# Optimization experiments

Hardware: AMD Instinct MI355X
Metric: run time of the kernel (lower is better)

The kernel has to match this reference:

```python
import jax, jax.numpy as jnp
import numpy as np

S, D, H, DK, DV = 2048, 1024, 16, 64, 64


def setup_inputs() -> dict:
    key = jax.random.key(0)
    ks = jax.random.split(key, 7)
    sc = 1.0 / np.sqrt(D)
    return {
        "encodings_for_q": jax.random.normal(ks[0], (S, D), jnp.float32),
        "encodings_for_k": jax.random.normal(ks[1], (S, D), jnp.float32),
        "encodings_for_v": jax.random.normal(ks[2], (S, D), jnp.float32),
        # per-head projection weights, stacked over heads (math-equivalent to
        # num_heads separate bias-free nn.Linear layers)
        "W_q": jax.random.normal(ks[3], (H, D, DK), jnp.float32) * sc,
        "W_k": jax.random.normal(ks[4], (H, D, DK), jnp.float32) * sc,
        "W_v": jax.random.normal(ks[5], (H, D, DV), jnp.float32) * sc,
        "W_out": jax.random.normal(ks[6], (H * DV, D), jnp.float32) * sc,
    }


def reference(encodings_for_q, encodings_for_k, encodings_for_v, W_q, W_k, W_v, W_out):
    # per-head projections: [H, S, dk/dv]
    q = jnp.einsum("sd,hdk->hsk", encodings_for_q, W_q)
    k = jnp.einsum("sd,hdk->hsk", encodings_for_k, W_k)
    v = jnp.einsum("sd,hdv->hsv", encodings_for_v, W_v)
    # scaled dot-product attention; scale = sqrt(d_k) (k.size(col_dim))
    sims = jnp.einsum("hsk,htk->hst", q, k) / jnp.sqrt(jnp.asarray(DK, q.dtype))
    attn = jax.nn.softmax(sims, axis=-1)
    ctx = jnp.einsum("hst,htv->hsv", attn, v)  # [H, S, dv]
    # concat heads along feature dim (head-major order, like torch.cat)
    cat = jnp.transpose(ctx, (1, 0, 2)).reshape(S, H * DV)
    return cat @ W_out
```

## Files before the change

kernel.cpp:

```cpp
#include <hip/hip_runtime.h>
#include <hip/hip_bf16.h>

typedef __attribute__((ext_vector_type(8))) short bf16x8;
typedef __attribute__((ext_vector_type(4))) float f32x4;

#define S_  2048
#define D_  1024
#define H_  16
#define QK_SCALE 0.18033688011f

__device__ __forceinline__ unsigned short f2bf(float x) {
    union { float f; unsigned u; } v; v.f = x;
    unsigned r = v.u + 0x7fffu + ((v.u >> 16) & 1u);
    return (unsigned short)(r >> 16);
}

__device__ __forceinline__ float bf2f(unsigned short s) {
    union { unsigned u; float f; } v; v.u = (unsigned)s << 16; return v.f;
}

__device__ __forceinline__ unsigned short bfbits(float x) {
    union { __hip_bfloat16 h; unsigned short s; } c;
    c.h = __float2bfloat16(x);
    return c.s;
}

__device__ __forceinline__ float fm3(float a, float b, float c) {
    return fmaxf(fmaxf(a, b), c);
}

__device__ __forceinline__ void gload16(const unsigned short* g, unsigned short* l) {
    __builtin_amdgcn_global_load_lds((const __attribute__((address_space(1))) void*)g,
                                     (__attribute__((address_space(3))) void*)l, 16, 0, 0);
}

__device__ __forceinline__ void drain_vm() {
    asm volatile("s_waitcnt vmcnt(0)" ::: "memory");
}

__global__ __launch_bounds__(256) void prep(
    const float* __restrict__ eq, const float* __restrict__ ek, const float* __restrict__ ev,
    const float* __restrict__ wq, const float* __restrict__ wk, const float* __restrict__ wv,
    const float* __restrict__ wo,
    unsigned short* __restrict__ oeq, unsigned short* __restrict__ oek,
    unsigned short* __restrict__ oev, unsigned short* __restrict__ owq,
    unsigned short* __restrict__ owk, unsigned short* __restrict__ owv,
    unsigned short* __restrict__ owo) {
    const int bx = blockIdx.x, tid = threadIdx.x;
    if (bx < 6144) {
        const float* in = bx < 2048 ? eq : bx < 4096 ? ek : ev;
        unsigned short* out = bx < 2048 ? oeq : bx < 4096 ? oek : oev;
        int i = (bx & 2047) * 256 + tid;
        float4 v = ((const float4*)in)[i];
        ushort4 o;
        o.x = f2bf(v.x); o.y = f2bf(v.y); o.z = f2bf(v.z); o.w = f2bf(v.w);
        ((ushort4*)out)[i] = o;
        return;
    }
    __shared__ float t[32][33];
    const int tx = tid & 31, ty = tid >> 5;
    if (bx < 9216) {
        int idx = bx - 6144;
        int zh = idx >> 6, rem = idx & 63;
        int which = zh >> 4, h = zh & 15;
        const float* I = (which == 0 ? wq : which == 1 ? wk : wv) + (long)h * 65536;
        unsigned short* O = (which == 0 ? owq : which == 1 ? owk : owv) + (long)h * 65536;
        float sc = which == 0 ? QK_SCALE : 1.0f;
        int c0 = (rem >> 5) * 32, r0 = (rem & 31) * 32;
        #pragma unroll
        for (int r = 0; r < 4; ++r)
            t[ty + r * 8][tx] = I[(long)(r0 + ty + r * 8) * 64 + c0 + tx];
        __syncthreads();
        #pragma unroll
        for (int r = 0; r < 4; ++r)
            O[(long)(c0 + ty + r * 8) * 1024 + r0 + tx] = f2bf(sc * t[tx][ty + r * 8]);
    } else {
        int idx = bx - 9216;
        int c0 = (idx >> 5) * 32, r0 = (idx & 31) * 32;
        #pragma unroll
        for (int r = 0; r < 4; ++r)
            t[ty + r * 8][tx] = wo[(long)(r0 + ty + r * 8) * 1024 + c0 + tx];
        __syncthreads();
        #pragma unroll
        for (int r = 0; r < 4; ++r)
            owo[(long)(c0 + ty + r * 8) * 1024 + r0 + tx] = f2bf(t[tx][ty + r * 8]);
    }
}

template<int MODE>
__device__ __forceinline__ void gemm64x128(unsigned short (*As)[64 * 64],
                                           unsigned short (*Bs)[128 * 64],
                                           const unsigned short* __restrict__ A,
                                           const unsigned short* __restrict__ Bt,
                                           void* __restrict__ C, int m0, int n0, int ldc) {
    const int tid = threadIdx.x, wv = tid >> 6, lane = tid & 63, lg = lane >> 4, lr = lane & 15;
    f32x4 acc[4][2] = {};
    const unsigned short* Ab = A + (size_t)m0 * D_;
    const unsigned short* Bb = Bt + (size_t)n0 * D_;
    auto stage = [&](int b, int kt) {
        #pragma unroll
        for (int it = 0; it < 2; ++it) {
            int c = it * 256 + wv * 64 + lane;
            int row = c >> 3, jj = (c & 7) ^ (row & 7);
            gload16(Ab + (size_t)row * D_ + kt * 64 + jj * 8, &As[b][(it * 256 + wv * 64) * 8]);
        }
        #pragma unroll
        for (int it = 0; it < 4; ++it) {
            int c = it * 256 + wv * 64 + lane;
            int row = c >> 3, jj = (c & 7) ^ (row & 7);
            gload16(Bb + (size_t)row * D_ + kt * 64 + jj * 8, &Bs[b][(it * 256 + wv * 64) * 8]);
        }
    };
    stage(0, 0);
    drain_vm();
    __syncthreads();
    int buf = 0;
    for (int kt = 0; kt < 16; ++kt) {
        if (kt + 1 < 16) stage(buf ^ 1, kt + 1);
        #pragma unroll
        for (int kk = 0; kk < 2; ++kk) {
            bf16x8 af[4], bfr[2];
            #pragma unroll
            for (int mf = 0; mf < 4; ++mf) {
                int r = mf * 16 + lr;
                af[mf] = *(const bf16x8*)&As[buf][(r * 8 + ((kk * 4 + lg) ^ (r & 7))) * 8];
            }
            #pragma unroll
            for (int nf = 0; nf < 2; ++nf) {
                int r = wv * 32 + nf * 16 + lr;
                bfr[nf] = *(const bf16x8*)&Bs[buf][(r * 8 + ((kk * 4 + lg) ^ (r & 7))) * 8];
            }
            #pragma unroll
            for (int mf = 0; mf < 4; ++mf)
                #pragma unroll
                for (int nf = 0; nf < 2; ++nf)
                    acc[mf][nf] = __builtin_amdgcn_mfma_f32_16x16x32_bf16(af[mf], bfr[nf], acc[mf][nf], 0, 0, 0);
        }
        drain_vm();
        __syncthreads();
        buf ^= 1;
    }
    #pragma unroll
    for (int mf = 0; mf < 4; ++mf)
        #pragma unroll
        for (int nf = 0; nf < 2; ++nf) {
            if (MODE == 1) {
                int gn = n0 + wv * 32 + nf * 16 + lr;
                int pg = m0 + (mf >> 1) * 32 + lg * 8 + (mf & 1) * 4;
                ushort4 pk;
                pk.x = f2bf(acc[mf][nf][0]); pk.y = f2bf(acc[mf][nf][1]);
                pk.z = f2bf(acc[mf][nf][2]); pk.w = f2bf(acc[mf][nf][3]);
                *(ushort4*)&((unsigned short*)C)[(size_t)gn * ldc + pg] = pk;
            } else {
                #pragma unroll
                for (int j = 0; j < 4; ++j) {
                    int gm = m0 + mf * 16 + lg * 4 + j;
                    int gn = n0 + wv * 32 + nf * 16 + lr;
                    ((unsigned short*)C)[(size_t)gm * ldc + gn] = f2bf(acc[mf][nf][j]);
                }
            }
        }
}

__global__ __launch_bounds__(256, 3) void proj_kernel(
    const unsigned short* __restrict__ Eq, const unsigned short* __restrict__ Ek,
    const unsigned short* __restrict__ Ev, const unsigned short* __restrict__ Wqt,
    const unsigned short* __restrict__ Wkt, const unsigned short* __restrict__ Wvt,
    unsigned short* __restrict__ Qb, unsigned short* __restrict__ Kb,
    unsigned short* __restrict__ Vtb) {
    __shared__ alignas(16) unsigned short As[2][64 * 64];
    __shared__ alignas(16) unsigned short Bs[2][128 * 64];
    int m0 = blockIdx.x * 64, n0 = blockIdx.y * 128;
    if (blockIdx.z == 0)      gemm64x128<0>(As, Bs, Eq, Wqt, Qb, m0, n0, 1024);
    else if (blockIdx.z == 1) gemm64x128<0>(As, Bs, Ek, Wkt, Kb, m0, n0, 1024);
    else                      gemm64x128<1>(As, Bs, Ev, Wvt, Vtb, m0, n0, S_);
}

__global__ __launch_bounds__(256, 2) void out_gemm(const unsigned short* __restrict__ Cat,
                                                   const unsigned short* __restrict__ Wot,
                                                   float* __restrict__ Out) {
    __shared__ alignas(16) unsigned short As[2][64 * 64];
    __shared__ alignas(16) unsigned short Bs[2][64 * 64];
    const int tid = threadIdx.x, wv = tid >> 6, lane = tid & 63, lg = lane >> 4, lr = lane & 15;
    int m0 = blockIdx.x * 64, n0 = blockIdx.y * 64;
    f32x4 acc[4] = {};
    const unsigned short* Ab = Cat + (size_t)m0 * D_;
    const unsigned short* Bb = Wot + (size_t)n0 * D_;
    auto stage = [&](int b, int kt) {
        #pragma unroll
        for (int it = 0; it < 2; ++it) {
            int c = it * 256 + wv * 64 + lane;
            int row = c >> 3, jj = (c & 7) ^ (row & 7);
            gload16(Ab + (size_t)row * D_ + kt * 64 + jj * 8, &As[b][(it * 256 + wv * 64) * 8]);
        }
        #pragma unroll
        for (int it = 0; it < 2; ++it) {
            int c = it * 256 + wv * 64 + lane;
            int row = c >> 3, jj = (c & 7) ^ (row & 7);
            gload16(Bb + (size_t)row * D_ + kt * 64 + jj * 8, &Bs[b][(it * 256 + wv * 64) * 8]);
        }
    };
    stage(0, 0);
    drain_vm();
    __syncthreads();
    int buf = 0;
    for (int kt = 0; kt < 16; ++kt) {
        if (kt + 1 < 16) stage(buf ^ 1, kt + 1);
        #pragma unroll
        for (int kk = 0; kk < 2; ++kk) {
            int ra = wv * 16 + lr;
            bf16x8 af = *(const bf16x8*)&As[buf][(ra * 8 + ((kk * 4 + lg) ^ (ra & 7))) * 8];
            #pragma unroll
            for (int nf = 0; nf < 4; ++nf) {
                int r = nf * 16 + lr;
                bf16x8 bfr = *(const bf16x8*)&Bs[buf][(r * 8 + ((kk * 4 + lg) ^ (r & 7))) * 8];
                acc[nf] = __builtin_amdgcn_mfma_f32_16x16x32_bf16(af, bfr, acc[nf], 0, 0, 0);
            }
        }
        drain_vm();
        __syncthreads();
        buf ^= 1;
    }
    #pragma unroll
    for (int nf = 0; nf < 4; ++nf)
        #pragma unroll
        for (int j = 0; j < 4; ++j)
            Out[(size_t)(m0 + wv * 16 + lg * 4 + j) * 1024 + n0 + nf * 16 + lr] = acc[nf][j];
}

__global__ __launch_bounds__(256, 3) void attn_kernel(
    const unsigned short* __restrict__ Qb, const unsigned short* __restrict__ Kb,
    const unsigned short* __restrict__ Vtb, unsigned short* __restrict__ Opb,
    float* __restrict__ Ml) {
    __shared__ alignas(16) unsigned short Ks[2][64 * 64];
    __shared__ alignas(16) unsigned short Vs[3][64 * 64];

    const int h = blockIdx.y, s0 = blockIdx.x * 128;
    const int tid = threadIdx.x, wv = tid >> 6, lane = tid & 63, lg = lane >> 4, lr = lane & 15;

    const unsigned short* qrA = Qb + (size_t)(s0 + wv * 32 + lr) * D_ + h * 64;
    const unsigned short* qrB = qrA + 16 * D_;
    const bf16x8 qA0 = *(const bf16x8*)(qrA + lg * 8);
    const bf16x8 qA1 = *(const bf16x8*)(qrA + 32 + lg * 8);
    const bf16x8 qB0 = *(const bf16x8*)(qrB + lg * 8);
    const bf16x8 qB1 = *(const bf16x8*)(qrB + 32 + lg * 8);

    float mA = 0.f, mB = 0.f, lA = 0.f, lB = 0.f;
    f32x4 oA[4] = {}, oB[4] = {};
    f32x4 sa[2][4], sb[2][4];

    const unsigned short* KhB = Kb + h * 64;
    const unsigned short* VhB = Vtb + (size_t)(h * 64) * S_;
    const int t0 = blockIdx.z * 8;

    auto stageL = [&](int u) {
        int t = t0 + u;
        #pragma unroll
        for (int it = 0; it < 2; ++it) {
            int c = it * 256 + wv * 64 + lane;
            int row = c >> 3, jj = (c & 7) ^ (row & 7);
            gload16(KhB + (size_t)(t * 64 + row) * D_ + jj * 8, &Ks[u & 1][(it * 256 + wv * 64) * 8]);
        }
        #pragma unroll
        for (int it = 0; it < 2; ++it) {
            int c = it * 256 + wv * 64 + lane;
            int row = c >> 3, jj = (c & 7) ^ (row & 7);
            gload16(VhB + (size_t)row * S_ + t * 64 + jj * 8, &Vs[u % 3][(it * 256 + wv * 64) * 8]);
        }
    };
    auto qk = [&](int u) {
        const unsigned short* K_ = Ks[u & 1];
        __builtin_amdgcn_s_setprio(1);
        #pragma unroll
        for (int kk = 0; kk < 2; ++kk) {
            bf16x8 qa = kk ? qA1 : qA0;
            bf16x8 qb = kk ? qB1 : qB0;
            #pragma unroll
            for (int n = 0; n < 4; ++n) {
                int r = n * 16 + lr;
                bf16x8 kf = *(const bf16x8*)&K_[(r * 8 + ((kk * 4 + lg) ^ (r & 7))) * 8];
                if (kk == 0) {
                    f32x4 z = {};
                    sa[u & 1][n] = __builtin_amdgcn_mfma_f32_16x16x32_bf16(kf, qa, z, 0, 0, 0);
                    sb[u & 1][n] = __builtin_amdgcn_mfma_f32_16x16x32_bf16(kf, qb, z, 0, 0, 0);
                } else {
                    sa[u & 1][n] = __builtin_amdgcn_mfma_f32_16x16x32_bf16(kf, qa, sa[u & 1][n], 0, 0, 0);
                    sb[u & 1][n] = __builtin_amdgcn_mfma_f32_16x16x32_bf16(kf, qb, sb[u & 1][n], 0, 0, 0);
                }
            }
        }
        __builtin_amdgcn_s_setprio(0);
    };

    stageL(0);
    stageL(1);
    #pragma unroll
    for (int tt = 0; tt < 8; ++tt) {
        __syncthreads();
        if (tt == 0) {
            qk(0);
            stageL(2);
        } else if (tt + 2 < 8) {
            stageL(tt + 2);
        }
        if (tt + 1 < 8) qk(tt + 1);

        f32x4* sA = sa[tt & 1];
        f32x4* sB = sb[tt & 1];
        float mxA, mxB;
        {
            float a0 = fm3(sA[0][0], sA[0][1], sA[0][2]);
            float a1 = fm3(sA[0][3], sA[1][0], sA[1][1]);
            float a2 = fm3(sA[1][2], sA[1][3], sA[2][0]);
            float a3 = fm3(sA[2][1], sA[2][2], sA[2][3]);
            float a4 = fm3(sA[3][0], sA[3][1], sA[3][2]);
            mxA = fm3(fm3(a0, a1, a2), fmaxf(a3, a4), sA[3][3]);
            float b0 = fm3(sB[0][0], sB[0][1], sB[0][2]);
            float b1 = fm3(sB[0][3], sB[1][0], sB[1][1]);
            float b2 = fm3(sB[1][2], sB[1][3], sB[2][0]);
            float b3 = fm3(sB[2][1], sB[2][2], sB[2][3]);
            float b4 = fm3(sB[3][0], sB[3][1], sB[3][2]);
            mxB = fm3(fm3(b0, b1, b2), fmaxf(b3, b4), sB[3][3]);
        }
        if (__any((mxA > mA + 11.f) || (mxB > mB + 11.f))) {
            mxA = fmaxf(mxA, __shfl_xor(mxA, 16)); mxA = fmaxf(mxA, __shfl_xor(mxA, 32));
            mxB = fmaxf(mxB, __shfl_xor(mxB, 16)); mxB = fmaxf(mxB, __shfl_xor(mxB, 32));
            float nA = fmaxf(mA, mxA), nB = fmaxf(mB, mxB);
            float aA = exp2f(mA - nA), aB = exp2f(mB - nB);
            mA = nA; mB = nB; lA *= aA; lB *= aB;
            #pragma unroll
            for (int n = 0; n < 4; ++n) { oA[n] *= aA; oB[n] *= aB; }
        }
        float rsA = 0.f, rsB = 0.f;
        #pragma unroll
        for (int n = 0; n < 4; ++n)
            #pragma unroll
            for (int j = 0; j < 4; ++j) {
                float pa = exp2f(sA[n][j] - mA);
                float pb = exp2f(sB[n][j] - mB);
                sA[n][j] = pa; rsA += pa;
                sB[n][j] = pb; rsB += pb;
            }
        lA += rsA; lB += rsB;

        bf16x8 pA[2], pB[2];
        #pragma unroll
        for (int kk = 0; kk < 2; ++kk) {
            union { bf16x8 v; unsigned short s[8]; } ua, ub;
            #pragma unroll
            for (int i = 0; i < 4; ++i) {
                ua.s[i]     = bfbits(sA[2 * kk][i]);
                ua.s[4 + i] = bfbits(sA[2 * kk + 1][i]);
                ub.s[i]     = bfbits(sB[2 * kk][i]);
                ub.s[4 + i] = bfbits(sB[2 * kk + 1][i]);
            }
            pA[kk] = ua.v; pB[kk] = ub.v;
        }
        const unsigned short* V_ = Vs[tt % 3];
        __builtin_amdgcn_s_setprio(1);
        #pragma unroll
        for (int n = 0; n < 4; ++n) {
            int r = n * 16 + lr;
            #pragma unroll
            for (int kk = 0; kk < 2; ++kk) {
                bf16x8 vf = *(const bf16x8*)&V_[(r * 8 + ((kk * 4 + lg) ^ (r & 7))) * 8];
                oA[n] = __builtin_amdgcn_mfma_f32_16x16x32_bf16(vf, pA[kk], oA[n], 0, 0, 0);
                oB[n] = __builtin_amdgcn_mfma_f32_16x16x32_bf16(vf, pB[kk], oB[n], 0, 0, 0);
            }
        }
        __builtin_amdgcn_s_setprio(0);
    }
    lA += __shfl_xor(lA, 16); lA += __shfl_xor(lA, 32);
    lB += __shfl_xor(lB, 16); lB += __shfl_xor(lB, 32);

    const int slot = blockIdx.z * 16 + h;
    size_t qa = (size_t)s0 + wv * 32 + lr, qb = qa + 16;
    size_t baseA = ((size_t)slot * S_ + qa) * 64;
    size_t baseB = ((size_t)slot * S_ + qb) * 64;
    #pragma unroll
    for (int n = 0; n < 4; ++n) {
        ushort4 ka, kb2;
        ka.x  = f2bf(oA[n][0]); ka.y  = f2bf(oA[n][1]);
        ka.z  = f2bf(oA[n][2]); ka.w  = f2bf(oA[n][3]);
        kb2.x = f2bf(oB[n][0]); kb2.y = f2bf(oB[n][1]);
        kb2.z = f2bf(oB[n][2]); kb2.w = f2bf(oB[n][3]);
        *(ushort4*)&Opb[baseA + n * 16 + lg * 4] = ka;
        *(ushort4*)&Opb[baseB + n * 16 + lg * 4] = kb2;
    }
    if (lg == 0) {
        size_t miA = (size_t)slot * S_ + qa, miB = (size_t)slot * S_ + qb;
        Ml[miA * 2] = mA; Ml[miA * 2 + 1] = lA;
        Ml[miB * 2] = mB; Ml[miB * 2 + 1] = lB;
    }
}

__global__ __launch_bounds__(256) void combine(const unsigned short* __restrict__ Opb,
                                               const float* __restrict__ Ml,
                                               unsigned short* __restrict__ Cat) {
    int gid = blockIdx.x * 256 + threadIdx.x;
    int d4 = gid & 15, s = (gid >> 4) & 2047, h = gid >> 15;
    float m[4], l[4];
    #pragma unroll
    for (int i = 0; i < 4; ++i) {
        size_t mi = ((size_t)(i * 16 + h) * S_ + s) * 2;
        m[i] = Ml[mi]; l[i] = Ml[mi + 1];
    }
    float M = fmaxf(fmaxf(m[0], m[1]), fmaxf(m[2], m[3]));
    float w[4], denom = 0.f;
    #pragma unroll
    for (int i = 0; i < 4; ++i) { w[i] = exp2f(m[i] - M); denom += w[i] * l[i]; }
    float inv = 1.f / fmaxf(denom, 1e-30f);
    float o0 = 0.f, o1 = 0.f, o2 = 0.f, o3 = 0.f;
    #pragma unroll
    for (int i = 0; i < 4; ++i) {
        ushort4 u = *(const ushort4*)&Opb[((size_t)(i * 16 + h) * S_ + s) * 64 + d4 * 4];
        o0 += w[i] * bf2f(u.x); o1 += w[i] * bf2f(u.y);
        o2 += w[i] * bf2f(u.z); o3 += w[i] * bf2f(u.w);
    }
    ushort4 pk;
    pk.x = f2bf(o0 * inv); pk.y = f2bf(o1 * inv);
    pk.z = f2bf(o2 * inv); pk.w = f2bf(o3 * inv);
    *(ushort4*)&Cat[(size_t)s * D_ + h * 64 + d4 * 4] = pk;
}

extern "C" void kernel_launch(void* const* d_in, const int* in_sizes, int n_in,
                              void* d_out, int out_size, void* d_ws, size_t ws_size,
                              hipStream_t stream) {
    const float* enc_q = (const float*)d_in[0];
    const float* enc_k = (const float*)d_in[1];
    const float* enc_v = (const float*)d_in[2];
    const float* W_q   = (const float*)d_in[3];
    const float* W_k   = (const float*)d_in[4];
    const float* W_v   = (const float*)d_in[5];
    const float* W_out = (const float*)d_in[6];
    float* out = (float*)d_out;

    const size_t M1 = 1024 * 1024;
    unsigned short* Eqb = (unsigned short*)d_ws;
    unsigned short* Ekb = Eqb + 2 * M1;
    unsigned short* Evb = Ekb + 2 * M1;
    unsigned short* Wqt = Evb + 2 * M1;
    unsigned short* Wkt = Wqt + M1;
    unsigned short* Wvt = Wkt + M1;
    unsigned short* Wot = Wvt + M1;
    unsigned short* Qb  = Wot + M1;
    unsigned short* Kb  = Qb  + 2 * M1;
    unsigned short* Vtb = Kb  + 2 * M1;
    unsigned short* Cat = Vtb + 2 * M1;
    unsigned short* Opb = (unsigned short*)d_ws;
    float* Ml = (float*)((char*)d_ws + 17u * 1024 * 1024);

    prep<<<10240, 256, 0, stream>>>(enc_q, enc_k, enc_v, W_q, W_k, W_v, W_out,
                                    Eqb, Ekb, Evb, Wqt, Wkt, Wvt, Wot);
    proj_kernel<<<dim3(32, 8, 3), 256, 0, stream>>>(Eqb, Ekb, Evb, Wqt, Wkt, Wvt, Qb, Kb, Vtb);
    attn_kernel<<<dim3(16, 16, 4), 256, 0, stream>>>(Qb, Kb, Vtb, Opb, Ml);
    combine<<<2048, 256, 0, stream>>>(Opb, Ml, Cat);
    out_gemm<<<dim3(32, 16), 256, 0, stream>>>(Cat, Wot, out);
}
```

Before: 93.45 us.

## Double attention block size and remap blocks for K/V sharing across XCDs

Each attention workgroup grows from 256 to 512 threads and covers 256 query rows, so every staged K/V tile in LDS is reused by twice as many waves and each thread issues one load per tile instead of two. The grid is flattened to a 1D launch and block IDs are remapped so that blocks with the same (head, key split) land on the same XCD (id mod 8), aiming to improve L2 locality for the K and V data. An extra barrier is added after the first QK step so that staging tile 2 cannot overwrite the V buffer early. The launch bound changes to (512,4), which may squeeze registers, and there are fewer blocks overall.

After: 115.1 us. 1.23x slower.

```diff
diff --git a/kernel.cpp b/kernel.cpp
--- a/kernel.cpp
+++ b/kernel.cpp
@@ -228,14 +228,19 @@
             Out[(size_t)(m0 + wv * 16 + lg * 4 + j) * 1024 + n0 + nf * 16 + lr] = acc[nf][j];
 }
 
-__global__ __launch_bounds__(256, 3) void attn_kernel(
+__global__ __launch_bounds__(512, 4) void attn_kernel(
     const unsigned short* __restrict__ Qb, const unsigned short* __restrict__ Kb,
     const unsigned short* __restrict__ Vtb, unsigned short* __restrict__ Opb,
     float* __restrict__ Ml) {
     __shared__ alignas(16) unsigned short Ks[2][64 * 64];
     __shared__ alignas(16) unsigned short Vs[3][64 * 64];
 
-    const int h = blockIdx.y, s0 = blockIdx.x * 128;
+    const int wgid = blockIdx.x;
+    const int g = wgid & 7, idx = wgid >> 3;
+    const int x = idx & 7, c = g + 8 * (idx >> 3);
+    const int h = c & 15, z = c >> 4;
+    const int s0 = x * 256;
+
     const int tid = threadIdx.x, wv = tid >> 6, lane = tid & 63, lg = lane >> 4, lr = lane & 15;
 
     const unsigned short* qrA = Qb + (size_t)(s0 + wv * 32 + lr) * D_ + h * 64;
@@ -251,22 +256,13 @@
 
     const unsigned short* KhB = Kb + h * 64;
     const unsigned short* VhB = Vtb + (size_t)(h * 64) * S_;
-    const int t0 = blockIdx.z * 8;
-
+    const int t0 = z * 8;
+
+    const int srow = tid >> 3, sjj = (tid & 7) ^ (srow & 7);
     auto stageL = [&](int u) {
         int t = t0 + u;
-        #pragma unroll
-        for (int it = 0; it < 2; ++it) {
-            int c = it * 256 + wv * 64 + lane;
-            int row = c >> 3, jj = (c & 7) ^ (row & 7);
-            gload16(KhB + (size_t)(t * 64 + row) * D_ + jj * 8, &Ks[u & 1][(it * 256 + wv * 64) * 8]);
-        }
-        #pragma unroll
-        for (int it = 0; it < 2; ++it) {
-            int c = it * 256 + wv * 64 + lane;
-            int row = c >> 3, jj = (c & 7) ^ (row & 7);
-            gload16(VhB + (size_t)row * S_ + t * 64 + jj * 8, &Vs[u % 3][(it * 256 + wv * 64) * 8]);
-        }
+        gload16(KhB + (size_t)(t * 64 + srow) * D_ + sjj * 8, &Ks[u & 1][(wv * 64) * 8]);
+        gload16(VhB + (size_t)srow * S_ + t * 64 + sjj * 8, &Vs[u % 3][(wv * 64) * 8]);
     };
     auto qk = [&](int u) {
         const unsigned short* K_ = Ks[u & 1];
@@ -280,9 +276,9 @@
                 int r = n * 16 + lr;
                 bf16x8 kf = *(const bf16x8*)&K_[(r * 8 + ((kk * 4 + lg) ^ (r & 7))) * 8];
                 if (kk == 0) {
-                    f32x4 z = {};
-                    sa[u & 1][n] = __builtin_amdgcn_mfma_f32_16x16x32_bf16(kf, qa, z, 0, 0, 0);
-                    sb[u & 1][n] = __builtin_amdgcn_mfma_f32_16x16x32_bf16(kf, qb, z, 0, 0, 0);
+                    f32x4 zz = {};
+                    sa[u & 1][n] = __builtin_amdgcn_mfma_f32_16x16x32_bf16(kf, qa, zz, 0, 0, 0);
+                    sb[u & 1][n] = __builtin_amdgcn_mfma_f32_16x16x32_bf16(kf, qb, zz, 0, 0, 0);
                 } else {
                     sa[u & 1][n] = __builtin_amdgcn_mfma_f32_16x16x32_bf16(kf, qa, sa[u & 1][n], 0, 0, 0);
                     sb[u & 1][n] = __builtin_amdgcn_mfma_f32_16x16x32_bf16(kf, qb, sb[u & 1][n], 0, 0, 0);
@@ -299,6 +295,7 @@
         __syncthreads();
         if (tt == 0) {
             qk(0);
+            __syncthreads();
             stageL(2);
         } else if (tt + 2 < 8) {
             stageL(tt + 2);
@@ -373,7 +370,7 @@
     lA += __shfl_xor(lA, 16); lA += __shfl_xor(lA, 32);
     lB += __shfl_xor(lB, 16); lB += __shfl_xor(lB, 32);
 
-    const int slot = blockIdx.z * 16 + h;
+    const int slot = z * 16 + h;
     size_t qa = (size_t)s0 + wv * 32 + lr, qb = qa + 16;
     size_t baseA = ((size_t)slot * S_ + qa) * 64;
     size_t baseB = ((size_t)slot * S_ + qb) * 64;
@@ -453,7 +450,7 @@
     prep<<<10240, 256, 0, stream>>>(enc_q, enc_k, enc_v, W_q, W_k, W_v, W_out,
                                     Eqb, Ekb, Evb, Wqt, Wkt, Wvt, Wot);
     proj_kernel<<<dim3(32, 8, 3), 256, 0, stream>>>(Eqb, Ekb, Evb, Wqt, Wkt, Wvt, Qb, Kb, Vtb);
-    attn_kernel<<<dim3(16, 16, 4), 256, 0, stream>>>(Qb, Kb, Vtb, Opb, Ml);
+    attn_kernel<<<512, 512, 0, stream>>>(Qb, Kb, Vtb, Opb, Ml);
     combine<<<2048, 256, 0, stream>>>(Opb, Ml, Cat);
     out_gemm<<<dim3(32, 16), 256, 0, stream>>>(Cat, Wot, out);
 }
```

## Double query rows per attention block and triple-buffer K tiles

Applied to the files above, without the earlier changes.

Each wave now processes 64 query rows (four 16-row strips) instead of 32, so every K and V fragment read from LDS feeds four MFMAs rather than two. This halves the grid along the sequence dimension. The cross-iteration QK-ahead software pipeline is replaced by a triple-buffered K ring with explicit vmcnt waits and raw barriers. Register pressure rises, so launch bounds drop to 2 blocks per CU. The grid shrinks to 512 blocks, and overlap of QK with softmax is lost.

Result: slower. 119.9 us (+28.3%).

```diff
diff --git a/kernel.cpp b/kernel.cpp
--- a/kernel.cpp
+++ b/kernel.cpp
@@ -228,30 +228,32 @@
             Out[(size_t)(m0 + wv * 16 + lg * 4 + j) * 1024 + n0 + nf * 16 + lr] = acc[nf][j];
 }
 
-__global__ __launch_bounds__(256, 3) void attn_kernel(
+__global__ __launch_bounds__(256, 2) void attn_kernel(
     const unsigned short* __restrict__ Qb, const unsigned short* __restrict__ Kb,
     const unsigned short* __restrict__ Vtb, unsigned short* __restrict__ Opb,
     float* __restrict__ Ml) {
-    __shared__ alignas(16) unsigned short Ks[2][64 * 64];
+    __shared__ alignas(16) unsigned short Ks[3][64 * 64];
     __shared__ alignas(16) unsigned short Vs[3][64 * 64];
 
-    const int h = blockIdx.y, s0 = blockIdx.x * 128;
+    const int h = blockIdx.y, s0 = blockIdx.x * 256, z = blockIdx.z;
     const int tid = threadIdx.x, wv = tid >> 6, lane = tid & 63, lg = lane >> 4, lr = lane & 15;
 
-    const unsigned short* qrA = Qb + (size_t)(s0 + wv * 32 + lr) * D_ + h * 64;
-    const unsigned short* qrB = qrA + 16 * D_;
-    const bf16x8 qA0 = *(const bf16x8*)(qrA + lg * 8);
-    const bf16x8 qA1 = *(const bf16x8*)(qrA + 32 + lg * 8);
-    const bf16x8 qB0 = *(const bf16x8*)(qrB + lg * 8);
-    const bf16x8 qB1 = *(const bf16x8*)(qrB + 32 + lg * 8);
-
-    float mA = 0.f, mB = 0.f, lA = 0.f, lB = 0.f;
-    f32x4 oA[4] = {}, oB[4] = {};
-    f32x4 sa[2][4], sb[2][4];
+    bf16x8 q0[4], q1[4];
+    #pragma unroll
+    for (int st = 0; st < 4; ++st) {
+        const unsigned short* qr = Qb + (size_t)(s0 + wv * 64 + st * 16 + lr) * D_ + h * 64;
+        q0[st] = *(const bf16x8*)(qr + lg * 8);
+        q1[st] = *(const bf16x8*)(qr + 32 + lg * 8);
+    }
+
+    float m[4], l[4];
+    #pragma unroll
+    for (int st = 0; st < 4; ++st) { m[st] = 0.f; l[st] = 0.f; }
+    f32x4 o[4][4] = {};
 
     const unsigned short* KhB = Kb + h * 64;
     const unsigned short* VhB = Vtb + (size_t)(h * 64) * S_;
-    const int t0 = blockIdx.z * 8;
+    const int t0 = z * 8;
 
     auto stageL = [&](int u) {
         int t = t0 + u;
@@ -259,7 +261,7 @@
         for (int it = 0; it < 2; ++it) {
             int c = it * 256 + wv * 64 + lane;
             int row = c >> 3, jj = (c & 7) ^ (row & 7);
-            gload16(KhB + (size_t)(t * 64 + row) * D_ + jj * 8, &Ks[u & 1][(it * 256 + wv * 64) * 8]);
+            gload16(KhB + (size_t)(t * 64 + row) * D_ + jj * 8, &Ks[u % 3][(it * 256 + wv * 64) * 8]);
         }
         #pragma unroll
         for (int it = 0; it < 2; ++it) {
@@ -268,95 +270,92 @@
             gload16(VhB + (size_t)row * S_ + t * 64 + jj * 8, &Vs[u % 3][(it * 256 + wv * 64) * 8]);
         }
     };
-    auto qk = [&](int u) {
-        const unsigned short* K_ = Ks[u & 1];
+
+    stageL(0);
+    stageL(1);
+    #pragma unroll
+    for (int tt = 0; tt < 8; ++tt) {
+        __builtin_amdgcn_s_barrier();
+        if (tt + 2 < 8) {
+            stageL(tt + 2);
+            asm volatile("s_waitcnt vmcnt(4)" ::: "memory");
+        } else {
+            asm volatile("s_waitcnt vmcnt(0)" ::: "memory");
+        }
+        __builtin_amdgcn_s_barrier();
+
+        const unsigned short* K_ = Ks[tt % 3];
+        const unsigned short* V_ = Vs[tt % 3];
+
+        f32x4 s[4][4];
         __builtin_amdgcn_s_setprio(1);
         #pragma unroll
-        for (int kk = 0; kk < 2; ++kk) {
-            bf16x8 qa = kk ? qA1 : qA0;
-            bf16x8 qb = kk ? qB1 : qB0;
+        for (int kk = 0; kk < 2; ++kk)
             #pragma unroll
             for (int n = 0; n < 4; ++n) {
                 int r = n * 16 + lr;
                 bf16x8 kf = *(const bf16x8*)&K_[(r * 8 + ((kk * 4 + lg) ^ (r & 7))) * 8];
-                if (kk == 0) {
-                    f32x4 z = {};
-                    sa[u & 1][n] = __builtin_amdgcn_mfma_f32_16x16x32_bf16(kf, qa, z, 0, 0, 0);
-                    sb[u & 1][n] = __builtin_amdgcn_mfma_f32_16x16x32_bf16(kf, qb, z, 0, 0, 0);
-                } else {
-                    sa[u & 1][n] = __builtin_amdgcn_mfma_f32_16x16x32_bf16(kf, qa, sa[u & 1][n], 0, 0, 0);
-                    sb[u & 1][n] = __builtin_amdgcn_mfma_f32_16x16x32_bf16(kf, qb, sb[u & 1][n], 0, 0, 0);
+                #pragma unroll
+                for (int st = 0; st < 4; ++st) {
+                    if (kk == 0) {
+                        f32x4 zz = {};
+                        s[st][n] = __builtin_amdgcn_mfma_f32_16x16x32_bf16(kf, q0[st], zz, 0, 0, 0);
+                    } else {
+                        s[st][n] = __builtin_amdgcn_mfma_f32_16x16x32_bf16(kf, q1[st], s[st][n], 0, 0, 0);
+                    }
                 }
             }
-        }
         __builtin_amdgcn_s_setprio(0);
-    };
-
-    stageL(0);
-    stageL(1);
-    #pragma unroll
-    for (int tt = 0; tt < 8; ++tt) {
-        __syncthreads();
-        if (tt == 0) {
-            qk(0);
-            stageL(2);
-        } else if (tt + 2 < 8) {
-            stageL(tt + 2);
-        }
-        if (tt + 1 < 8) qk(tt + 1);
-
-        f32x4* sA = sa[tt & 1];
-        f32x4* sB = sb[tt & 1];
-        float mxA, mxB;
-        {
-            float a0 = fm3(sA[0][0], sA[0][1], sA[0][2]);
-            float a1 = fm3(sA[0][3], sA[1][0], sA[1][1]);
-            float a2 = fm3(sA[1][2], sA[1][3], sA[2][0]);
-            float a3 = fm3(sA[2][1], sA[2][2], sA[2][3]);
-            float a4 = fm3(sA[3][0], sA[3][1], sA[3][2]);
-            mxA = fm3(fm3(a0, a1, a2), fmaxf(a3, a4), sA[3][3]);
-            float b0 = fm3(sB[0][0], sB[0][1], sB[0][2]);
-            float b1 = fm3(sB[0][3], sB[1][0], sB[1][1]);
-            float b2 = fm3(sB[1][2], sB[1][3], sB[2][0]);
-            float b3 = fm3(sB[2][1], sB[2][2], sB[2][3]);
-            float b4 = fm3(sB[3][0], sB[3][1], sB[3][2]);
-            mxB = fm3(fm3(b0, b1, b2), fmaxf(b3, b4), sB[3][3]);
-        }
-        if (__any((mxA > mA + 11.f) || (mxB > mB + 11.f))) {
-            mxA = fmaxf(mxA, __shfl_xor(mxA, 16)); mxA = fmaxf(mxA, __shfl_xor(mxA, 32));
-            mxB = fmaxf(mxB, __shfl_xor(mxB, 16)); mxB = fmaxf(mxB, __shfl_xor(mxB, 32));
-            float nA = fmaxf(mA, mxA), nB = fmaxf(mB, mxB);
-            float aA = exp2f(mA - nA), aB = exp2f(mB - nB);
-            mA = nA; mB = nB; lA *= aA; lB *= aB;
-            #pragma unroll
-            for (int n = 0; n < 4; ++n) { oA[n] *= aA; oB[n] *= aB; }
-        }
-        float rsA = 0.f, rsB = 0.f;
-        #pragma unroll
-        for (int n = 0; n < 4; ++n)
-            #pragma unroll
-            for (int j = 0; j < 4; ++j) {
-                float pa = exp2f(sA[n][j] - mA);
-                float pb = exp2f(sB[n][j] - mB);
-                sA[n][j] = pa; rsA += pa;
-                sB[n][j] = pb; rsB += pb;
-            }
-        lA += rsA; lB += rsB;
-
-        bf16x8 pA[2], pB[2];
-        #pragma unroll
-        for (int kk = 0; kk < 2; ++kk) {
-            union { bf16x8 v; unsigned short s[8]; } ua, ub;
-            #pragma unroll
-            for (int i = 0; i < 4; ++i) {
-                ua.s[i]     = bfbits(sA[2 * kk][i]);
-                ua.s[4 + i] = bfbits(sA[2 * kk + 1][i]);
-                ub.s[i]     = bfbits(sB[2 * kk][i]);
-                ub.s[4 + i] = bfbits(sB[2 * kk + 1][i]);
-            }
-            pA[kk] = ua.v; pB[kk] = ub.v;
-        }
-        const unsigned short* V_ = Vs[tt % 3];
+
+        float mx[4];
+        #pragma unroll
+        for (int st = 0; st < 4; ++st) {
+            float a0 = fm3(s[st][0][0], s[st][0][1], s[st][0][2]);
+            float a1 = fm3(s[st][0][3], s[st][1][0], s[st][1][1]);
+            float a2 = fm3(s[st][1][2], s[st][1][3], s[st][2][0]);
+            float a3 = fm3(s[st][2][1], s[st][2][2], s[st][2][3]);
+            float a4 = fm3(s[st][3][0], s[st][3][1], s[st][3][2]);
+            mx[st] = fm3(fm3(a0, a1, a2), fmaxf(a3, a4), s[st][3][3]);
+        }
+        bool fire = (mx[0] > m[0] + 11.f) || (mx[1] > m[1] + 11.f) ||
+                    (mx[2] > m[2] + 11.f) || (mx[3] > m[3] + 11.f);
+        if (__any(fire)) {
+            #pragma unroll
+            for (int st = 0; st < 4; ++st) {
+                float v = mx[st];
+                v = fmaxf(v, __shfl_xor(v, 16)); v = fmaxf(v, __shfl_xor(v, 32));
+                float nm = fmaxf(m[st], v);
+                float al = exp2f(m[st] - nm);
+                m[st] = nm; l[st] *= al;
+                #pragma unroll
+                for (int n = 0; n < 4; ++n) o[st][n] *= al;
+            }
+        }
+        #pragma unroll
+        for (int st = 0; st < 4; ++st) {
+            float rs = 0.f;
+            #pragma unroll
+            for (int n = 0; n < 4; ++n)
+                #pragma unroll
+                for (int j = 0; j < 4; ++j) {
+                    float p = exp2f(s[st][n][j] - m[st]);
+                    s[st][n][j] = p; rs += p;
+                }
+            l[st] += rs;
+        }
+        bf16x8 p[4][2];
+        #pragma unroll
+        for (int st = 0; st < 4; ++st)
+            #pragma unroll
+            for (int kk = 0; kk < 2; ++kk) {
+                union { bf16x8 v; unsigned short u[8]; } t_;
+                #pragma unroll
+                for (int i = 0; i < 4; ++i) {
+                    t_.u[i]     = bfbits(s[st][2 * kk][i]);
+                    t_.u[4 + i] = bfbits(s[st][2 * kk + 1][i]);
+                }
+                p[st][kk] = t_.v;
+            }
         __builtin_amdgcn_s_setprio(1);
         #pragma unroll
         for (int n = 0; n < 4; ++n) {
@@ -364,33 +363,34 @@
             #pragma unroll
             for (int kk = 0; kk < 2; ++kk) {
                 bf16x8 vf = *(const bf16x8*)&V_[(r * 8 + ((kk * 4 + lg) ^ (r & 7))) * 8];
-                oA[n] = __builtin_amdgcn_mfma_f32_16x16x32_bf16(vf, pA[kk], oA[n], 0, 0, 0);
-                oB[n] = __builtin_amdgcn_mfma_f32_16x16x32_bf16(vf, pB[kk], oB[n], 0, 0, 0);
+                #pragma unroll
+                for (int st = 0; st < 4; ++st)
+                    o[st][n] = __builtin_amdgcn_mfma_f32_16x16x32_bf16(vf, p[st][kk], o[st][n], 0, 0, 0);
             }
         }
         __builtin_amdgcn_s_setprio(0);
     }
-    lA += __shfl_xor(lA, 16); lA += __shfl_xor(lA, 32);
-    lB += __shfl_xor(lB, 16); lB += __shfl_xor(lB, 32);
-
-    const int slot = blockIdx.z * 16 + h;
-    size_t qa = (size_t)s0 + wv * 32 + lr, qb = qa + 16;
-    size_t baseA = ((size_t)slot * S_ + qa) * 64;
-    size_t baseB = ((size_t)slot * S_ + qb) * 64;
-    #pragma unroll
-    for (int n = 0; n < 4; ++n) {
-        ushort4 ka, kb2;
-        ka.x  = f2bf(oA[n][0]); ka.y  = f2bf(oA[n][1]);
-        ka.z  = f2bf(oA[n][2]); ka.w  = f2bf(oA[n][3]);
-        kb2.x = f2bf(oB[n][0]); kb2.y = f2bf(oB[n][1]);
-        kb2.z = f2bf(oB[n][2]); kb2.w = f2bf(oB[n][3]);
-        *(ushort4*)&Opb[baseA + n * 16 + lg * 4] = ka;
-        *(ushort4*)&Opb[baseB + n * 16 + lg * 4] = kb2;
-    }
-    if (lg == 0) {
-        size_t miA = (size_t)slot * S_ + qa, miB = (size_t)slot * S_ + qb;
-        Ml[miA * 2] = mA; Ml[miA * 2 + 1] = lA;
-        Ml[miB * 2] = mB; Ml[miB * 2 + 1] = lB;
+    #pragma unroll
+    for (int st = 0; st < 4; ++st) {
+        l[st] += __shfl_xor(l[st], 16);
+        l[st] += __shfl_xor(l[st], 32);
+    }
+    const int slot = z * 16 + h;
+    #pragma unroll
+    for (int st = 0; st < 4; ++st) {
+        size_t q = (size_t)s0 + wv * 64 + st * 16 + lr;
+        size_t base = ((size_t)slot * S_ + q) * 64;
+        #pragma unroll
+        for (int n = 0; n < 4; ++n) {
+            ushort4 pk;
+            pk.x = f2bf(o[st][n][0]); pk.y = f2bf(o[st][n][1]);
+            pk.z = f2bf(o[st][n][2]); pk.w = f2bf(o[st][n][3]);
+            *(ushort4*)&Opb[base + n * 16 + lg * 4] = pk;
+        }
+        if (lg == 0) {
+            size_t mi = (size_t)slot * S_ + q;
+            Ml[mi * 2] = m[st]; Ml[mi * 2 + 1] = l[st];
+        }
     }
 }
 
@@ -453,7 +453,7 @@
     prep<<<10240, 256, 0, stream>>>(enc_q, enc_k, enc_v, W_q, W_k, W_v, W_out,
                                     Eqb, Ekb, Evb, Wqt, Wkt, Wvt, Wot);
     proj_kernel<<<dim3(32, 8, 3), 256, 0, stream>>>(Eqb, Ekb, Evb, Wqt, Wkt, Wvt, Qb, Kb, Vtb);
-    attn_kernel<<<dim3(16, 16, 4), 256, 0, stream>>>(Qb, Kb, Vtb, Opb, Ml);
+    attn_kernel<<<dim3(8, 16, 4), 256, 0, stream>>>(Qb, Kb, Vtb, Opb, Ml);
     combine<<<2048, 256, 0, stream>>>(Opb, Ml, Cat);
     out_gemm<<<dim3(32, 16), 256, 0, stream>>>(Cat, Wot, out);
 }
```
